# Kernel optimization log

Hardware: AMD Instinct MI355X
Metric: run time of the kernel (lower is better)

Reference implementation:

```python
import jax, jax.numpy as jnp
import numpy as np

N_AGENTS = 32
STATE_DIM = 6 * N_AGENTS      # 192
CONTROL_DIM = 3 * N_AGENTS    # 96
HIDDEN = 100
NEWTON_ITERS = 40

# Index maps from the cvxpy objective:
#   p[u_x_r]^T u[u_idx] + p[u_y_r]^T u[2*u_idx] + p[u_z_r]^T u[3*u_idx]
_u_idx = np.arange(N_AGENTS)
P_IDX = np.concatenate([3 * np.arange(1, N_AGENTS + 1),
                        4 * np.arange(1, N_AGENTS + 1),
                        5 * np.arange(1, N_AGENTS + 1)])
U_IDX = np.concatenate([_u_idx, 2 * _u_idx, 3 * _u_idx])


def _p_net(t, z, W1, b1, W2, b2, W3, b3):
    # DefaultPNet: MLP on concat([t, z]) with tanh hiddens (hidden_dim=100)
    x = jnp.concatenate([t, z], axis=-1)          # [B, 1+STATE_DIM]
    h = jnp.tanh(x @ W1 + b1)
    h = jnp.tanh(h @ W2 + b2)
    return h @ W3 + b3                            # [B, STATE_DIM]


def _solve_qp(q):
    # min_u q^T u + 0.5||u||^2 + 0.25||u||^4  (unconstrained, strictly convex)
    # Stationarity: q + (1+||u||^2) u = 0 => u = -q/(1+s), s = ||u||^2
    # => s (1+s)^2 = ||q||^2 ; solve scalar cubic per row via Newton.
    r = jnp.sum(q * q, axis=-1)                   # [B]
    s0 = jnp.cbrt(r)                              # good init: s ~ r^(1/3) for large r

    def step(s, _):
        one = 1.0 + s
        f = s * one * one - r
        fp = one * one + 2.0 * s * one
        return jnp.maximum(s - f / fp, 0.0), None

    s, _ = jax.lax.scan(step, s0, None, length=NEWTON_ITERS)
    return -q / (1.0 + s)[:, None]                # [B, CONTROL_DIM]


def setup_inputs() -> dict:
    key = jax.random.key(0)
    ks = jax.random.split(key, 8)
    B = 131072
    in_dim = 1 + STATE_DIM
    sc1 = 1.0 / np.sqrt(in_dim)
    sc2 = 1.0 / np.sqrt(HIDDEN)
    return {
        "z": jax.random.normal(ks[0], (B, STATE_DIM), jnp.float32),
        "t": jax.random.uniform(ks[1], (B, 1), jnp.float32),
        "W1": jax.random.normal(ks[2], (in_dim, HIDDEN), jnp.float32) * sc1,
        "b1": jnp.zeros((HIDDEN,), jnp.float32),
        "W2": jax.random.normal(ks[3], (HIDDEN, HIDDEN), jnp.float32) * sc2,
        "b2": jnp.zeros((HIDDEN,), jnp.float32),
        "W3": jax.random.normal(ks[4], (HIDDEN, STATE_DIM), jnp.float32) * sc2,
        "b3": jnp.zeros((STATE_DIM,), jnp.float32),
    }


def reference(z, t, W1, b1, W2, b2, W3, b3):
    p = _p_net(t, z, W1, b1, W2, b2, W3, b3)      # [B, STATE_DIM]
    # Accumulate linear coefficients onto u (indices overlap, so scatter-add)
    q = jnp.zeros((p.shape[0], CONTROL_DIM), p.dtype).at[:, U_IDX].add(p[:, P_IDX])
    return _solve_qp(q)                            # ustar [B, CONTROL_DIM]
```

## Files before the change

### kernel.cpp

```cpp
#include <hip/hip_runtime.h>
#include <hip/hip_bf16.h>


typedef __attribute__((ext_vector_type(8))) short short8;
typedef __attribute__((ext_vector_type(4))) short short4v;
typedef __attribute__((ext_vector_type(4))) float f32x4;

#define HST 116

__device__ __forceinline__ unsigned short f2bf(float f) {
  unsigned u = __float_as_uint(f);
  u += 0x7fffu + ((u >> 16) & 1u);
  return (unsigned short)(u >> 16);
}
__device__ __forceinline__ float tanh_fast(float x) {
  float ax = fabsf(x);
  float e = __builtin_amdgcn_exp2f(ax * -2.88539008177792681f);
  float r = (1.f - e) * __builtin_amdgcn_rcpf(1.f + e);
  return copysignf(r, x);
}
__device__ __forceinline__ short8 pack_bf8(f32x4 a, f32x4 b) {
  union { short8 s; __hip_bfloat162 h[4]; } u;
  u.h[0] = __float22bfloat162_rn(make_float2(a[0], a[1]));
  u.h[1] = __float22bfloat162_rn(make_float2(a[2], a[3]));
  u.h[2] = __float22bfloat162_rn(make_float2(b[0], b[1]));
  u.h[3] = __float22bfloat162_rn(make_float2(b[2], b[3]));
  return u.s;
}

__global__ void cvx_prep(const float* __restrict__ W1, const float* __restrict__ b1,
                         const float* __restrict__ W2, const float* __restrict__ b2,
                         const float* __restrict__ W3, const float* __restrict__ b3,
                         short* __restrict__ pw) {
  int idx = blockIdx.x * 256 + threadIdx.x;

  if (idx < 21504) {
    int kt = idx / 3584, rem = idx % 3584;
    int nt = rem / 512, e = rem % 512;
    int lane = e >> 3, j = e & 7;
    int k = kt * 32 + (lane >> 4) * 8 + j;
    int n = nt * 16 + (lane & 15);
    float wv = (n < 100) ? W1[(k + 1) * 100 + n] : 0.f;
    pw[(kt * 7 + nt) * 512 + e] = (short)f2bf(wv);
    return;
  }
  idx -= 21504;
  if (idx < 14336) {
    int kt = idx / 3584, rem = idx % 3584;
    int nt = rem / 512, e = rem % 512;
    int lane = e >> 3, j = e & 7;
    int k = kt * 32 + (lane >> 4) * 8 + j;
    int n = nt * 16 + (lane & 15);
    float wv = (k < 100 && n < 100) ? W2[k * 100 + n] : 0.f;
    pw[21504 + (kt * 7 + nt) * 512 + e] = (short)f2bf(wv);
    return;
  }
  idx -= 14336;
  if (idx < 12288) {
    int kt = idx / 3072, rem = idx % 3072;
    int nt = rem / 512, e = rem % 512;
    int lane = e >> 3, j = e & 7;
    int k = kt * 32 + (lane >> 4) * 8 + j;
    int u = nt * 16 + (lane & 15);
    float wv = 0.f;
    if (k < 100) {
      const float* wr = W3 + k * 192;
      if (u <= 31) wv += wr[3 * u + 3];
      if ((u & 1) == 0 && u <= 62) wv += wr[2 * u + 4];
      if (u % 3 == 0 && u <= 93) wv += wr[(5 * u) / 3 + 5];
    }
    pw[35840 + (kt * 6 + nt) * 512 + e] = (short)f2bf(wv);
    return;
  }
  idx -= 12288;
  float* cb = (float*)(pw + 48128);
  if (idx < 112) { cb[idx] = (idx < 100) ? W1[idx] : 0.f; return; }
  idx -= 112;
  if (idx < 112) { cb[112 + idx] = (idx < 100) ? b1[idx] : 0.f; return; }
  idx -= 112;
  if (idx < 112) { cb[224 + idx] = (idx < 100) ? b2[idx] : 0.f; return; }
  idx -= 112;
  if (idx < 96) {
    int u = idx;
    float v = 0.f;
    if (u <= 31) v += b3[3 * u + 3];
    if ((u & 1) == 0 && u <= 62) v += b3[2 * u + 4];
    if (u % 3 == 0 && u <= 93) v += b3[(5 * u) / 3 + 5];
    cb[336 + u] = v;
  }
}

__global__ __launch_bounds__(512, 2) void cvx_main(
    const float* __restrict__ zin, const float* __restrict__ tin,
    const short* __restrict__ pw, float* __restrict__ out) {
  __shared__ __align__(16) short wbuf[48128];
  __shared__ __align__(16) short hbuf[8 * 32 * HST];
  __shared__ __align__(16) float cbl[448];

  const int tid = threadIdx.x;
  const int wid = tid >> 6;
  const int lane = tid & 63;
  const int l15 = lane & 15;
  const int qd = lane >> 4;

  for (int f = wid; f < 94; f += 8) {
    const short* g = pw + f * 512 + lane * 8;
    __builtin_amdgcn_global_load_lds(
        (const __attribute__((address_space(1))) void*)g,
        (__attribute__((address_space(3))) void*)&wbuf[f * 512], 16, 0, 0);
  }
  if (tid < 448) cbl[tid] = ((const float*)(pw + 48128))[tid];

  const int row0 = blockIdx.x * 512 + wid * 32;
  const int hb = wid * 32 * HST;

  short8 XA[2][6];
  float tc0, tc1;
#pragma unroll
  for (int mt = 0; mt < 2; mt++) {
    const float* zr = zin + (size_t)(row0 + mt * 16 + l15) * 192 + qd * 8;
#pragma unroll
    for (int kt = 0; kt < 6; kt++) {
      f32x4 a = *(const f32x4*)(zr + kt * 32);
      f32x4 b = *(const f32x4*)(zr + kt * 32 + 4);
      XA[mt][kt] = pack_bf8(a, b);
    }
  }
  tc0 = tin[row0 + l15];
  tc1 = tin[row0 + 16 + l15];

  __syncthreads();

  auto ldh = [&](int off) -> short8 {
    short4v a = *(const short4v*)&hbuf[off];
    short4v b = *(const short4v*)&hbuf[off + 4];
    return __builtin_shufflevector(a, b, 0, 1, 2, 3, 4, 5, 6, 7);
  };

  short8 XN[2][6];
  float tn0, tn1;

#pragma unroll 1
  for (int ii = 0; ii < 2; ++ii) {
    const int rb = row0 + ii * 256;

    f32x4 acc[2][7];
#pragma unroll
    for (int nt = 0; nt < 7; nt++) {
      f32x4 zzz = {0.f, 0.f, 0.f, 0.f};
      acc[0][nt] = zzz; acc[1][nt] = zzz;
    }

    f32x4 sg[2][2][2];
    const float* zb = zin + (size_t)(row0 + 256 + l15) * 192 + qd * 8;

    if (ii == 0) {
#pragma unroll
      for (int mt = 0; mt < 2; mt++)
#pragma unroll
        for (int kp = 0; kp < 2; kp++) {
          sg[mt][kp][0] = *(const f32x4*)(zb + mt * 3072 + kp * 32);
          sg[mt][kp][1] = *(const f32x4*)(zb + mt * 3072 + kp * 32 + 4);
        }
      __builtin_amdgcn_sched_barrier(0);
    }

#pragma unroll
    for (int kt = 0; kt < 2; kt++)
#pragma unroll
      for (int nt = 0; nt < 7; nt++) {
        short8 bf = *(const short8*)&wbuf[(kt * 7 + nt) * 512 + lane * 8];
        acc[0][nt] = __builtin_amdgcn_mfma_f32_16x16x32_bf16(XA[0][kt], bf, acc[0][nt], 0, 0, 0);
        acc[1][nt] = __builtin_amdgcn_mfma_f32_16x16x32_bf16(XA[1][kt], bf, acc[1][nt], 0, 0, 0);
      }

    if (ii == 0) {
#pragma unroll
      for (int mt = 0; mt < 2; mt++)
#pragma unroll
        for (int kp = 0; kp < 2; kp++)
          XN[mt][kp] = pack_bf8(sg[mt][kp][0], sg[mt][kp][1]);
#pragma unroll
      for (int mt = 0; mt < 2; mt++)
#pragma unroll
        for (int kp = 0; kp < 2; kp++) {
          sg[mt][kp][0] = *(const f32x4*)(zb + mt * 3072 + (2 + kp) * 32);
          sg[mt][kp][1] = *(const f32x4*)(zb + mt * 3072 + (2 + kp) * 32 + 4);
        }
      __builtin_amdgcn_sched_barrier(0);
    }

#pragma unroll
    for (int kt = 2; kt < 4; kt++)
#pragma unroll
      for (int nt = 0; nt < 7; nt++) {
        short8 bf = *(const short8*)&wbuf[(kt * 7 + nt) * 512 + lane * 8];
        acc[0][nt] = __builtin_amdgcn_mfma_f32_16x16x32_bf16(XA[0][kt], bf, acc[0][nt], 0, 0, 0);
        acc[1][nt] = __builtin_amdgcn_mfma_f32_16x16x32_bf16(XA[1][kt], bf, acc[1][nt], 0, 0, 0);
      }

    if (ii == 0) {
#pragma unroll
      for (int mt = 0; mt < 2; mt++)
#pragma unroll
        for (int kp = 0; kp < 2; kp++)
          XN[mt][2 + kp] = pack_bf8(sg[mt][kp][0], sg[mt][kp][1]);
#pragma unroll
      for (int mt = 0; mt < 2; mt++)
#pragma unroll
        for (int kp = 0; kp < 2; kp++) {
          sg[mt][kp][0] = *(const f32x4*)(zb + mt * 3072 + (4 + kp) * 32);
          sg[mt][kp][1] = *(const f32x4*)(zb + mt * 3072 + (4 + kp) * 32 + 4);
        }
      tn0 = tin[row0 + 256 + l15];
      tn1 = tin[row0 + 256 + 16 + l15];
      __builtin_amdgcn_sched_barrier(0);
    }

#pragma unroll
    for (int kt = 4; kt < 6; kt++)
#pragma unroll
      for (int nt = 0; nt < 7; nt++) {
        short8 bf = *(const short8*)&wbuf[(kt * 7 + nt) * 512 + lane * 8];
        acc[0][nt] = __builtin_amdgcn_mfma_f32_16x16x32_bf16(XA[0][kt], bf, acc[0][nt], 0, 0, 0);
        acc[1][nt] = __builtin_amdgcn_mfma_f32_16x16x32_bf16(XA[1][kt], bf, acc[1][nt], 0, 0, 0);
      }

    float tr[2][4];
#pragma unroll
    for (int r = 0; r < 4; r++) {
      tr[0][r] = __shfl(tc0, qd * 4 + r);
      tr[1][r] = __shfl(tc1, qd * 4 + r);
    }
#pragma unroll
    for (int nt = 0; nt < 7; nt++) {
      float w0v = cbl[nt * 16 + l15];
      float b1v = cbl[112 + nt * 16 + l15];
#pragma unroll
      for (int mt = 0; mt < 2; mt++)
#pragma unroll
        for (int r = 0; r < 4; r++) {
          float v = fmaf(tr[mt][r], w0v, acc[mt][nt][r] + b1v);
          hbuf[hb + (mt * 16 + qd * 4 + r) * HST + nt * 16 + l15] = (short)f2bf(tanh_fast(v));
        }
    }

    if (ii == 0) {
#pragma unroll
      for (int mt = 0; mt < 2; mt++)
#pragma unroll
        for (int kp = 0; kp < 2; kp++)
          XN[mt][4 + kp] = pack_bf8(sg[mt][kp][0], sg[mt][kp][1]);
    }

    short8 HA[2][4];
#pragma unroll
    for (int mt = 0; mt < 2; mt++) {
      int ro = hb + (mt * 16 + l15) * HST;
#pragma unroll
      for (int kt = 0; kt < 3; kt++) HA[mt][kt] = ldh(ro + kt * 32 + qd * 8);
      HA[mt][3] = ldh(ro + 96 + (qd & 1) * 8);
    }
#pragma unroll
    for (int nt = 0; nt < 7; nt++) {
      f32x4 zzz = {0.f, 0.f, 0.f, 0.f};
      acc[0][nt] = zzz; acc[1][nt] = zzz;
    }
#pragma unroll
    for (int kt = 0; kt < 4; kt++)
#pragma unroll
      for (int nt = 0; nt < 7; nt++) {
        short8 bf = *(const short8*)&wbuf[(42 + kt * 7 + nt) * 512 + lane * 8];
        acc[0][nt] = __builtin_amdgcn_mfma_f32_16x16x32_bf16(HA[0][kt], bf, acc[0][nt], 0, 0, 0);
        acc[1][nt] = __builtin_amdgcn_mfma_f32_16x16x32_bf16(HA[1][kt], bf, acc[1][nt], 0, 0, 0);
      }
#pragma unroll
    for (int nt = 0; nt < 7; nt++) {
      float b2v = cbl[224 + nt * 16 + l15];
#pragma unroll
      for (int mt = 0; mt < 2; mt++)
#pragma unroll
        for (int r = 0; r < 4; r++) {
          float v = acc[mt][nt][r] + b2v;
          hbuf[hb + (mt * 16 + qd * 4 + r) * HST + nt * 16 + l15] = (short)f2bf(tanh_fast(v));
        }
    }

#pragma unroll
    for (int mt = 0; mt < 2; mt++) {
      int ro = hb + (mt * 16 + l15) * HST;
#pragma unroll
      for (int kt = 0; kt < 3; kt++) HA[mt][kt] = ldh(ro + kt * 32 + qd * 8);
      HA[mt][3] = ldh(ro + 96 + (qd & 1) * 8);
    }
    f32x4 qa[2][6];
#pragma unroll
    for (int nt = 0; nt < 6; nt++) {
      f32x4 zzz = {0.f, 0.f, 0.f, 0.f};
      qa[0][nt] = zzz; qa[1][nt] = zzz;
    }
#pragma unroll
    for (int kt = 0; kt < 4; kt++)
#pragma unroll
      for (int nt = 0; nt < 6; nt++) {
        short8 bf = *(const short8*)&wbuf[(70 + kt * 6 + nt) * 512 + lane * 8];
        qa[0][nt] = __builtin_amdgcn_mfma_f32_16x16x32_bf16(HA[0][kt], bf, qa[0][nt], 0, 0, 0);
        qa[1][nt] = __builtin_amdgcn_mfma_f32_16x16x32_bf16(HA[1][kt], bf, qa[1][nt], 0, 0, 0);
      }

#pragma unroll
    for (int mt = 0; mt < 2; mt++) {
#pragma unroll
      for (int nt = 0; nt < 6; nt++) {
        float bq = cbl[336 + nt * 16 + l15];
        qa[mt][nt][0] += bq; qa[mt][nt][1] += bq;
        qa[mt][nt][2] += bq; qa[mt][nt][3] += bq;
      }
      f32x4 rs = {0.f, 0.f, 0.f, 0.f};
#pragma unroll
      for (int nt = 0; nt < 6; nt++) rs += qa[mt][nt] * qa[mt][nt];
      float rv[4];
#pragma unroll
      for (int r = 0; r < 4; r++) {
        float v = rs[r];
        v += __shfl_xor(v, 1);
        v += __shfl_xor(v, 2);
        v += __shfl_xor(v, 4);
        v += __shfl_xor(v, 8);
        rv[r] = v;
      }
      float r2 = rv[l15 & 3];
      float s = __builtin_amdgcn_exp2f(__builtin_amdgcn_logf(r2) * 0.333333333333f);
#pragma unroll
      for (int itn = 0; itn < 8; itn++) {
        float one = 1.f + s;
        float fv = fmaf(s * one, one, -r2);
        float fp = one * fmaf(2.f, s, one);
        s = fmaxf(s - fv * __builtin_amdgcn_rcpf(fp), 0.f);
      }
      float myinv = -__builtin_amdgcn_rcpf(1.f + s);
#pragma unroll
      for (int r = 0; r < 4; r++) {
        float inv = __shfl(myinv, (lane & 48) | r);
        float* orow = out + (size_t)(rb + mt * 16 + qd * 4 + r) * 96;
#pragma unroll
        for (int nt = 0; nt < 6; nt++)
          orow[nt * 16 + l15] = qa[mt][nt][r] * inv;
      }
    }

    if (ii == 0) {
#pragma unroll
      for (int mt = 0; mt < 2; mt++)
#pragma unroll
        for (int kt = 0; kt < 6; kt++) XA[mt][kt] = XN[mt][kt];
      tc0 = tn0; tc1 = tn1;
    }
  }
}

extern "C" void kernel_launch(void* const* d_in, const int* in_sizes, int n_in,
                              void* d_out, int out_size, void* d_ws, size_t ws_size,
                              hipStream_t stream) {
  const float* z  = (const float*)d_in[0];
  const float* t  = (const float*)d_in[1];
  const float* W1 = (const float*)d_in[2];
  const float* b1 = (const float*)d_in[3];
  const float* W2 = (const float*)d_in[4];
  const float* b2 = (const float*)d_in[5];
  const float* W3 = (const float*)d_in[6];
  const float* b3 = (const float*)d_in[7];
  float* out = (float*)d_out;
  int B = in_sizes[0] / 192;

  short* pw = (short*)d_ws;
  cvx_prep<<<190, 256, 0, stream>>>(W1, b1, W2, b2, W3, b3, pw);
  cvx_main<<<B / 512, 512, 0, stream>>>(z, t, pw, out);
}
```

Measured before the change: 190.7 us.

## Transpose MFMA operands and pass hidden activations via lane shuffles instead of LDS

Swaps the MFMA operand order so weights are the A operand and activations the B operand. Each lane's accumulator then holds four consecutive hidden features of one batch row. Hidden activations are packed to bf16 in registers and redistributed with cross-lane shuffles to form the next layer's operand, which removes the LDS hbuf round trip and its barriers. Bias loads and output stores become 16-byte vectors, and the row norm needs only two shuffles. The cost is many extra shuffle and select instructions plus higher register pressure.

```diff
diff --git a/kernel.cpp b/kernel.cpp
--- a/kernel.cpp
+++ b/kernel.cpp
@@ -3,10 +3,7 @@
 
 
 typedef __attribute__((ext_vector_type(8))) short short8;
-typedef __attribute__((ext_vector_type(4))) short short4v;
 typedef __attribute__((ext_vector_type(4))) float f32x4;
-
-#define HST 116
 
 __device__ __forceinline__ unsigned short f2bf(float f) {
   unsigned u = __float_as_uint(f);
@@ -26,6 +23,11 @@
   u.h[2] = __float22bfloat162_rn(make_float2(b[0], b[1]));
   u.h[3] = __float22bfloat162_rn(make_float2(b[2], b[3]));
   return u.s;
+}
+__device__ __forceinline__ unsigned pk2u(float lo, float hi) {
+  union { __hip_bfloat162 h; unsigned u; } x;
+  x.h = __float22bfloat162_rn(make_float2(lo, hi));
+  return x.u;
 }
 
 __global__ void cvx_prep(const float* __restrict__ W1, const float* __restrict__ b1,
@@ -94,7 +96,6 @@
     const float* __restrict__ zin, const float* __restrict__ tin,
     const short* __restrict__ pw, float* __restrict__ out) {
   __shared__ __align__(16) short wbuf[48128];
-  __shared__ __align__(16) short hbuf[8 * 32 * HST];
   __shared__ __align__(16) float cbl[448];
 
   const int tid = threadIdx.x;
@@ -102,6 +103,9 @@
   const int lane = tid & 63;
   const int l15 = lane & 15;
   const int qd = lane >> 4;
+  const int lo_src = ((lane & 16) << 1) + l15;
+  const int hi_src = lo_src + 16;
+  const bool selA = lane < 32;
 
   for (int f = wid; f < 94; f += 8) {
     const short* g = pw + f * 512 + lane * 8;
@@ -112,18 +116,17 @@
   if (tid < 448) cbl[tid] = ((const float*)(pw + 48128))[tid];
 
   const int row0 = blockIdx.x * 512 + wid * 32;
-  const int hb = wid * 32 * HST;
-
-  short8 XA[2][6];
+
+  short8 XB[2][6];
   float tc0, tc1;
 #pragma unroll
-  for (int mt = 0; mt < 2; mt++) {
-    const float* zr = zin + (size_t)(row0 + mt * 16 + l15) * 192 + qd * 8;
+  for (int bt = 0; bt < 2; bt++) {
+    const float* zr = zin + (size_t)(row0 + bt * 16 + l15) * 192 + qd * 8;
 #pragma unroll
     for (int kt = 0; kt < 6; kt++) {
       f32x4 a = *(const f32x4*)(zr + kt * 32);
       f32x4 b = *(const f32x4*)(zr + kt * 32 + 4);
-      XA[mt][kt] = pack_bf8(a, b);
+      XB[bt][kt] = pack_bf8(a, b);
     }
   }
   tc0 = tin[row0 + l15];
@@ -131,10 +134,28 @@
 
   __syncthreads();
 
-  auto ldh = [&](int off) -> short8 {
-    short4v a = *(const short4v*)&hbuf[off];
-    short4v b = *(const short4v*)&hbuf[off + 4];
-    return __builtin_shufflevector(a, b, 0, 1, 2, 3, 4, 5, 6, 7);
+  auto buildHB = [&](const unsigned (&pkb)[7][2], int kt) -> short8 {
+    union { short8 s; unsigned u[4]; } hb;
+    if (kt < 3) {
+      unsigned a0 = (unsigned)__shfl((int)pkb[2 * kt][0], lo_src);
+      unsigned b0 = (unsigned)__shfl((int)pkb[2 * kt + 1][0], lo_src);
+      unsigned a1 = (unsigned)__shfl((int)pkb[2 * kt][1], lo_src);
+      unsigned b1_ = (unsigned)__shfl((int)pkb[2 * kt + 1][1], lo_src);
+      unsigned a2 = (unsigned)__shfl((int)pkb[2 * kt][0], hi_src);
+      unsigned b2_ = (unsigned)__shfl((int)pkb[2 * kt + 1][0], hi_src);
+      unsigned a3 = (unsigned)__shfl((int)pkb[2 * kt][1], hi_src);
+      unsigned b3_ = (unsigned)__shfl((int)pkb[2 * kt + 1][1], hi_src);
+      hb.u[0] = selA ? a0 : b0;
+      hb.u[1] = selA ? a1 : b1_;
+      hb.u[2] = selA ? a2 : b2_;
+      hb.u[3] = selA ? a3 : b3_;
+    } else {
+      hb.u[0] = (unsigned)__shfl((int)pkb[6][0], lo_src);
+      hb.u[1] = (unsigned)__shfl((int)pkb[6][1], lo_src);
+      hb.u[2] = (unsigned)__shfl((int)pkb[6][0], hi_src);
+      hb.u[3] = (unsigned)__shfl((int)pkb[6][1], hi_src);
+    }
+    return hb.s;
   };
 
   short8 XN[2][6];
@@ -156,11 +177,11 @@
 
     if (ii == 0) {
 #pragma unroll
-      for (int mt = 0; mt < 2; mt++)
+      for (int bt = 0; bt < 2; bt++)
 #pragma unroll
         for (int kp = 0; kp < 2; kp++) {
-          sg[mt][kp][0] = *(const f32x4*)(zb + mt * 3072 + kp * 32);
-          sg[mt][kp][1] = *(const f32x4*)(zb + mt * 3072 + kp * 32 + 4);
+          sg[bt][kp][0] = *(const f32x4*)(zb + bt * 3072 + kp * 32);
+          sg[bt][kp][1] = *(const f32x4*)(zb + bt * 3072 + kp * 32 + 4);
         }
       __builtin_amdgcn_sched_barrier(0);
     }
@@ -169,23 +190,23 @@
     for (int kt = 0; kt < 2; kt++)
 #pragma unroll
       for (int nt = 0; nt < 7; nt++) {
-        short8 bf = *(const short8*)&wbuf[(kt * 7 + nt) * 512 + lane * 8];
-        acc[0][nt] = __builtin_amdgcn_mfma_f32_16x16x32_bf16(XA[0][kt], bf, acc[0][nt], 0, 0, 0);
-        acc[1][nt] = __builtin_amdgcn_mfma_f32_16x16x32_bf16(XA[1][kt], bf, acc[1][nt], 0, 0, 0);
-      }
-
-    if (ii == 0) {
-#pragma unroll
-      for (int mt = 0; mt < 2; mt++)
+        short8 wf = *(const short8*)&wbuf[(kt * 7 + nt) * 512 + lane * 8];
+        acc[0][nt] = __builtin_amdgcn_mfma_f32_16x16x32_bf16(wf, XB[0][kt], acc[0][nt], 0, 0, 0);
+        acc[1][nt] = __builtin_amdgcn_mfma_f32_16x16x32_bf16(wf, XB[1][kt], acc[1][nt], 0, 0, 0);
+      }
+
+    if (ii == 0) {
+#pragma unroll
+      for (int bt = 0; bt < 2; bt++)
 #pragma unroll
         for (int kp = 0; kp < 2; kp++)
-          XN[mt][kp] = pack_bf8(sg[mt][kp][0], sg[mt][kp][1]);
-#pragma unroll
-      for (int mt = 0; mt < 2; mt++)
+          XN[bt][kp] = pack_bf8(sg[bt][kp][0], sg[bt][kp][1]);
+#pragma unroll
+      for (int bt = 0; bt < 2; bt++)
 #pragma unroll
         for (int kp = 0; kp < 2; kp++) {
-          sg[mt][kp][0] = *(const f32x4*)(zb + mt * 3072 + (2 + kp) * 32);
-          sg[mt][kp][1] = *(const f32x4*)(zb + mt * 3072 + (2 + kp) * 32 + 4);
+          sg[bt][kp][0] = *(const f32x4*)(zb + bt * 3072 + (2 + kp) * 32);
+          sg[bt][kp][1] = *(const f32x4*)(zb + bt * 3072 + (2 + kp) * 32 + 4);
         }
       __builtin_amdgcn_sched_barrier(0);
     }
@@ -194,23 +215,23 @@
     for (int kt = 2; kt < 4; kt++)
 #pragma unroll
       for (int nt = 0; nt < 7; nt++) {
-        short8 bf = *(const short8*)&wbuf[(kt * 7 + nt) * 512 + lane * 8];
-        acc[0][nt] = __builtin_amdgcn_mfma_f32_16x16x32_bf16(XA[0][kt], bf, acc[0][nt], 0, 0, 0);
-        acc[1][nt] = __builtin_amdgcn_mfma_f32_16x16x32_bf16(XA[1][kt], bf, acc[1][nt], 0, 0, 0);
-      }
-
-    if (ii == 0) {
-#pragma unroll
-      for (int mt = 0; mt < 2; mt++)
+        short8 wf = *(const short8*)&wbuf[(kt * 7 + nt) * 512 + lane * 8];
+        acc[0][nt] = __builtin_amdgcn_mfma_f32_16x16x32_bf16(wf, XB[0][kt], acc[0][nt], 0, 0, 0);
+        acc[1][nt] = __builtin_amdgcn_mfma_f32_16x16x32_bf16(wf, XB[1][kt], acc[1][nt], 0, 0, 0);
+      }
+
+    if (ii == 0) {
+#pragma unroll
+      for (int bt = 0; bt < 2; bt++)
 #pragma unroll
         for (int kp = 0; kp < 2; kp++)
-          XN[mt][2 + kp] = pack_bf8(sg[mt][kp][0], sg[mt][kp][1]);
-#pragma unroll
-      for (int mt = 0; mt < 2; mt++)
+          XN[bt][2 + kp] = pack_bf8(sg[bt][kp][0], sg[bt][kp][1]);
+#pragma unroll
+      for (int bt = 0; bt < 2; bt++)
 #pragma unroll
         for (int kp = 0; kp < 2; kp++) {
-          sg[mt][kp][0] = *(const f32x4*)(zb + mt * 3072 + (4 + kp) * 32);
-          sg[mt][kp][1] = *(const f32x4*)(zb + mt * 3072 + (4 + kp) * 32 + 4);
+          sg[bt][kp][0] = *(const f32x4*)(zb + bt * 3072 + (4 + kp) * 32);
+          sg[bt][kp][1] = *(const f32x4*)(zb + bt * 3072 + (4 + kp) * 32 + 4);
         }
       tn0 = tin[row0 + 256 + l15];
       tn1 = tin[row0 + 256 + 16 + l15];
@@ -221,78 +242,68 @@
     for (int kt = 4; kt < 6; kt++)
 #pragma unroll
       for (int nt = 0; nt < 7; nt++) {
-        short8 bf = *(const short8*)&wbuf[(kt * 7 + nt) * 512 + lane * 8];
-        acc[0][nt] = __builtin_amdgcn_mfma_f32_16x16x32_bf16(XA[0][kt], bf, acc[0][nt], 0, 0, 0);
-        acc[1][nt] = __builtin_amdgcn_mfma_f32_16x16x32_bf16(XA[1][kt], bf, acc[1][nt], 0, 0, 0);
-      }
-
-    float tr[2][4];
-#pragma unroll
-    for (int r = 0; r < 4; r++) {
-      tr[0][r] = __shfl(tc0, qd * 4 + r);
-      tr[1][r] = __shfl(tc1, qd * 4 + r);
-    }
-#pragma unroll
-    for (int nt = 0; nt < 7; nt++) {
-      float w0v = cbl[nt * 16 + l15];
-      float b1v = cbl[112 + nt * 16 + l15];
-#pragma unroll
-      for (int mt = 0; mt < 2; mt++)
-#pragma unroll
-        for (int r = 0; r < 4; r++) {
-          float v = fmaf(tr[mt][r], w0v, acc[mt][nt][r] + b1v);
-          hbuf[hb + (mt * 16 + qd * 4 + r) * HST + nt * 16 + l15] = (short)f2bf(tanh_fast(v));
-        }
-    }
-
-    if (ii == 0) {
-#pragma unroll
-      for (int mt = 0; mt < 2; mt++)
+        short8 wf = *(const short8*)&wbuf[(kt * 7 + nt) * 512 + lane * 8];
+        acc[0][nt] = __builtin_amdgcn_mfma_f32_16x16x32_bf16(wf, XB[0][kt], acc[0][nt], 0, 0, 0);
+        acc[1][nt] = __builtin_amdgcn_mfma_f32_16x16x32_bf16(wf, XB[1][kt], acc[1][nt], 0, 0, 0);
+      }
+
+#pragma unroll
+    for (int bt = 0; bt < 2; bt++) {
+      float tcb = (bt == 0) ? tc0 : tc1;
+#pragma unroll
+      for (int nt = 0; nt < 7; nt++) {
+        f32x4 w0v = *(const f32x4*)&cbl[nt * 16 + qd * 4];
+        f32x4 b1v = *(const f32x4*)&cbl[112 + nt * 16 + qd * 4];
+#pragma unroll
+        for (int r = 0; r < 4; r++)
+          acc[bt][nt][r] = tanh_fast(fmaf(tcb, w0v[r], acc[bt][nt][r] + b1v[r]));
+      }
+    }
+    unsigned pk[2][7][2];
+#pragma unroll
+    for (int bt = 0; bt < 2; bt++)
+#pragma unroll
+      for (int nt = 0; nt < 7; nt++) {
+        pk[bt][nt][0] = pk2u(acc[bt][nt][0], acc[bt][nt][1]);
+        pk[bt][nt][1] = pk2u(acc[bt][nt][2], acc[bt][nt][3]);
+      }
+
+    if (ii == 0) {
+#pragma unroll
+      for (int bt = 0; bt < 2; bt++)
 #pragma unroll
         for (int kp = 0; kp < 2; kp++)
-          XN[mt][4 + kp] = pack_bf8(sg[mt][kp][0], sg[mt][kp][1]);
-    }
-
-    short8 HA[2][4];
-#pragma unroll
-    for (int mt = 0; mt < 2; mt++) {
-      int ro = hb + (mt * 16 + l15) * HST;
-#pragma unroll
-      for (int kt = 0; kt < 3; kt++) HA[mt][kt] = ldh(ro + kt * 32 + qd * 8);
-      HA[mt][3] = ldh(ro + 96 + (qd & 1) * 8);
-    }
+          XN[bt][4 + kp] = pack_bf8(sg[bt][kp][0], sg[bt][kp][1]);
+    }
+
 #pragma unroll
     for (int nt = 0; nt < 7; nt++) {
       f32x4 zzz = {0.f, 0.f, 0.f, 0.f};
       acc[0][nt] = zzz; acc[1][nt] = zzz;
     }
 #pragma unroll
-    for (int kt = 0; kt < 4; kt++)
-#pragma unroll
-      for (int nt = 0; nt < 7; nt++) {
-        short8 bf = *(const short8*)&wbuf[(42 + kt * 7 + nt) * 512 + lane * 8];
-        acc[0][nt] = __builtin_amdgcn_mfma_f32_16x16x32_bf16(HA[0][kt], bf, acc[0][nt], 0, 0, 0);
-        acc[1][nt] = __builtin_amdgcn_mfma_f32_16x16x32_bf16(HA[1][kt], bf, acc[1][nt], 0, 0, 0);
-      }
-#pragma unroll
-    for (int nt = 0; nt < 7; nt++) {
-      float b2v = cbl[224 + nt * 16 + l15];
-#pragma unroll
-      for (int mt = 0; mt < 2; mt++)
-#pragma unroll
-        for (int r = 0; r < 4; r++) {
-          float v = acc[mt][nt][r] + b2v;
-          hbuf[hb + (mt * 16 + qd * 4 + r) * HST + nt * 16 + l15] = (short)f2bf(tanh_fast(v));
-        }
-    }
-
-#pragma unroll
-    for (int mt = 0; mt < 2; mt++) {
-      int ro = hb + (mt * 16 + l15) * HST;
-#pragma unroll
-      for (int kt = 0; kt < 3; kt++) HA[mt][kt] = ldh(ro + kt * 32 + qd * 8);
-      HA[mt][3] = ldh(ro + 96 + (qd & 1) * 8);
-    }
+    for (int kt = 0; kt < 4; kt++) {
+      short8 hb0 = buildHB(pk[0], kt);
+      short8 hb1 = buildHB(pk[1], kt);
+#pragma unroll
+      for (int nt = 0; nt < 7; nt++) {
+        short8 wf = *(const short8*)&wbuf[(42 + kt * 7 + nt) * 512 + lane * 8];
+        acc[0][nt] = __builtin_amdgcn_mfma_f32_16x16x32_bf16(wf, hb0, acc[0][nt], 0, 0, 0);
+        acc[1][nt] = __builtin_amdgcn_mfma_f32_16x16x32_bf16(wf, hb1, acc[1][nt], 0, 0, 0);
+      }
+    }
+#pragma unroll
+    for (int bt = 0; bt < 2; bt++)
+#pragma unroll
+      for (int nt = 0; nt < 7; nt++) {
+        f32x4 b2v = *(const f32x4*)&cbl[224 + nt * 16 + qd * 4];
+#pragma unroll
+        for (int r = 0; r < 4; r++)
+          acc[bt][nt][r] = tanh_fast(acc[bt][nt][r] + b2v[r]);
+        pk[bt][nt][0] = pk2u(acc[bt][nt][0], acc[bt][nt][1]);
+        pk[bt][nt][1] = pk2u(acc[bt][nt][2], acc[bt][nt][3]);
+      }
+
     f32x4 qa[2][6];
 #pragma unroll
     for (int nt = 0; nt < 6; nt++) {
@@ -300,36 +311,33 @@
       qa[0][nt] = zzz; qa[1][nt] = zzz;
     }
 #pragma unroll
-    for (int kt = 0; kt < 4; kt++)
+    for (int kt = 0; kt < 4; kt++) {
+      short8 hb0 = buildHB(pk[0], kt);
+      short8 hb1 = buildHB(pk[1], kt);
 #pragma unroll
       for (int nt = 0; nt < 6; nt++) {
-        short8 bf = *(const short8*)&wbuf[(70 + kt * 6 + nt) * 512 + lane * 8];
-        qa[0][nt] = __builtin_amdgcn_mfma_f32_16x16x32_bf16(HA[0][kt], bf, qa[0][nt], 0, 0, 0);
-        qa[1][nt] = __builtin_amdgcn_mfma_f32_16x16x32_bf16(HA[1][kt], bf, qa[1][nt], 0, 0, 0);
-      }
-
-#pragma unroll
-    for (int mt = 0; mt < 2; mt++) {
+        short8 wf = *(const short8*)&wbuf[(70 + kt * 6 + nt) * 512 + lane * 8];
+        qa[0][nt] = __builtin_amdgcn_mfma_f32_16x16x32_bf16(wf, hb0, qa[0][nt], 0, 0, 0);
+        qa[1][nt] = __builtin_amdgcn_mfma_f32_16x16x32_bf16(wf, hb1, qa[1][nt], 0, 0, 0);
+      }
+    }
+
+#pragma unroll
+    for (int bt = 0; bt < 2; bt++) {
 #pragma unroll
       for (int nt = 0; nt < 6; nt++) {
-        float bq = cbl[336 + nt * 16 + l15];
-        qa[mt][nt][0] += bq; qa[mt][nt][1] += bq;
-        qa[mt][nt][2] += bq; qa[mt][nt][3] += bq;
-      }
-      f32x4 rs = {0.f, 0.f, 0.f, 0.f};
-#pragma unroll
-      for (int nt = 0; nt < 6; nt++) rs += qa[mt][nt] * qa[mt][nt];
-      float rv[4];
-#pragma unroll
-      for (int r = 0; r < 4; r++) {
-        float v = rs[r];
-        v += __shfl_xor(v, 1);
-        v += __shfl_xor(v, 2);
-        v += __shfl_xor(v, 4);
-        v += __shfl_xor(v, 8);
-        rv[r] = v;
-      }
-      float r2 = rv[l15 & 3];
+        f32x4 bqv = *(const f32x4*)&cbl[336 + nt * 16 + qd * 4];
+        qa[bt][nt] += bqv;
+      }
+      float loc = 0.f;
+#pragma unroll
+      for (int nt = 0; nt < 6; nt++) {
+        f32x4 q = qa[bt][nt];
+        loc += q[0] * q[0] + q[1] * q[1] + q[2] * q[2] + q[3] * q[3];
+      }
+      loc += __shfl_xor(loc, 16);
+      loc += __shfl_xor(loc, 32);
+      float r2 = loc;
       float s = __builtin_amdgcn_exp2f(__builtin_amdgcn_logf(r2) * 0.333333333333f);
 #pragma unroll
       for (int itn = 0; itn < 8; itn++) {
@@ -338,22 +346,20 @@
         float fp = one * fmaf(2.f, s, one);
         s = fmaxf(s - fv * __builtin_amdgcn_rcpf(fp), 0.f);
       }
-      float myinv = -__builtin_amdgcn_rcpf(1.f + s);
-#pragma unroll
-      for (int r = 0; r < 4; r++) {
-        float inv = __shfl(myinv, (lane & 48) | r);
-        float* orow = out + (size_t)(rb + mt * 16 + qd * 4 + r) * 96;
-#pragma unroll
-        for (int nt = 0; nt < 6; nt++)
-          orow[nt * 16 + l15] = qa[mt][nt][r] * inv;
-      }
-    }
-
-    if (ii == 0) {
-#pragma unroll
-      for (int mt = 0; mt < 2; mt++)
-#pragma unroll
-        for (int kt = 0; kt < 6; kt++) XA[mt][kt] = XN[mt][kt];
+      float inv = -__builtin_amdgcn_rcpf(1.f + s);
+      float* orow = out + (size_t)(rb + bt * 16 + l15) * 96;
+#pragma unroll
+      for (int nt = 0; nt < 6; nt++) {
+        f32x4 v = qa[bt][nt] * inv;
+        *(f32x4*)(orow + nt * 16 + qd * 4) = v;
+      }
+    }
+
+    if (ii == 0) {
+#pragma unroll
+      for (int bt = 0; bt < 2; bt++)
+#pragma unroll
+        for (int kt = 0; kt < 6; kt++) XB[bt][kt] = XN[bt][kt];
       tc0 = tn0; tc1 = tn1;
     }
   }
```

Result: no change. 192.3 us (+0.8%).
